# Kernel optimization log

Measured on AMD Instinct MI355X. Metric: run time of the kernel, lower is better.

Reference implementation:

```python
import jax, jax.numpy as jnp
import numpy as np

B, C, H, W = 64, 256, 16, 16
HEADS, HEAD_DIM = 8, 256            # NOTE: source code requires H*W == HEAD_DIM
HID = HEADS * HEAD_DIM              # 2048
TEMB = 512
EPS = 1e-6
SC = HEAD_DIM ** -0.5


def setup_inputs() -> dict:
    key = jax.random.key(0)
    ks = jax.random.split(key, 6)
    return {
        "x": jax.random.normal(ks[0], (B, C, H, W), jnp.float32),
        "time_emb": jax.random.normal(ks[1], (B, TEMB), jnp.float32),
        "mlp_w": jax.random.normal(ks[2], (2 * C, TEMB), jnp.float32) * 0.02,
        "mlp_b": jnp.zeros((2 * C,), jnp.float32),
        "qkv_w": jax.random.normal(ks[3], (3 * HID, C), jnp.float32) * 0.02,
        "out_w": jax.random.normal(ks[4], (C, HID), jnp.float32) * 0.02,
        "out_b": jnp.zeros((C,), jnp.float32),
        "out_norm_scale": jnp.ones((C,), jnp.float32),
    }


def reference(x, time_emb, mlp_w, mlp_b, qkv_w, out_w, out_b, out_norm_scale):
    # AdaRMSNorm: SiLU -> Linear -> per-batch (scale, shift) over channels
    ss = jax.nn.silu(time_emb) @ mlp_w.T + mlp_b          # [B, 2C]
    scale, shift = jnp.split(ss, 2, axis=1)
    scale = scale[:, :, None, None]
    shift = shift[:, :, None, None]
    inv = jax.lax.rsqrt(jnp.mean(x * x, axis=1, keepdims=True) + EPS)
    xn = x * inv * (1.0 + scale) + shift

    # 1x1 conv producing q,k,v
    qkv = jnp.einsum('bchw,oc->bohw', xn, qkv_w)          # [B, 3*HID, H, W]
    q, k, v = jnp.split(qkv, 3, axis=1)

    def to_heads(t):
        return t.reshape(B, HEADS, HEAD_DIM, H * W)       # [B, h, d, L]

    q = jax.nn.softmax(to_heads(q), axis=2) * SC          # softmax over head_dim
    k = jax.nn.softmax(to_heads(k), axis=3)               # softmax over spatial
    v = to_heads(v)

    # Faithful to source einsums (contract over head_dim c, then over c and lw1)
    ctx = jnp.einsum('bhcn,bhcm->bhnm', k, v) * SC        # [B, h, L, L]
    out = jnp.einsum('bhnm,bhcl->bhml', ctx, q)           # [B, h, L, L]

    # rearrange 'b h c (l w) -> b (h c) l w' (valid since L == HEAD_DIM)
    out = out.reshape(B, HID, H, W)

    # output 1x1 conv + RMSNorm + residual
    y = jnp.einsum('bohw,co->bchw', out, out_w) + out_b[None, :, None, None]
    inv2 = jax.lax.rsqrt(jnp.mean(y * y, axis=1, keepdims=True) + EPS)
    y = y * inv2 * out_norm_scale[None, :, None, None]
    return y + x
```

## Files before the change

kernel.cpp:

```cpp
#include <hip/hip_runtime.h>
#include <math.h>


static constexpr float EPSV = 1e-6f;
static constexpr float SC2 = 1.0f / 256.0f;

__device__ __forceinline__ float wave_sum(float v) {
    v += __shfl_xor(v, 1);  v += __shfl_xor(v, 2);
    v += __shfl_xor(v, 4);  v += __shfl_xor(v, 8);
    v += __shfl_xor(v, 16); v += __shfl_xor(v, 32);
    return v;
}

__global__ void __launch_bounds__(256) k0_prep(
    const float* __restrict__ temb, const float* __restrict__ mlp_w,
    const float* __restrict__ mlp_b, const float* __restrict__ qkv_w,
    float* __restrict__ scsh, float* __restrict__ wvg)
{
    const int blk = blockIdx.x, tid = threadIdx.x;
    const int wv = tid >> 6, lane = tid & 63;
    if (blk < 1024) {
        int b = blk >> 4, jg = blk & 15;
        __shared__ float sl[512];
        float v0 = temb[b * 512 + tid];
        float v1 = temb[b * 512 + 256 + tid];
        sl[tid] = v0 / (1.0f + expf(-v0));
        sl[256 + tid] = v1 / (1.0f + expf(-v1));
        __syncthreads();
        int j0 = jg * 32 + wv * 8;
        float acc[8] = {0, 0, 0, 0, 0, 0, 0, 0};
        const float* wb = mlp_w + (size_t)j0 * 512 + lane;
#pragma unroll
        for (int k = 0; k < 8; ++k) {
            float sv = sl[k * 64 + lane];
#pragma unroll
            for (int jj = 0; jj < 8; ++jj)
                acc[jj] = fmaf(wb[(size_t)jj * 512 + k * 64], sv, acc[jj]);
        }
#pragma unroll
        for (int jj = 0; jj < 8; ++jj) {
            float a = wave_sum(acc[jj]);
            if (lane == 0) scsh[b * 512 + j0 + jj] = a + mlp_b[j0 + jj];
        }
    } else {
        int w = blk - 1024;
        int h = w >> 2, cq = w & 3;
        __shared__ float sm[256];
        const float* base =
            qkv_w + (size_t)(4096 + h * 256 + wv * 64) * 256 + cq * 64 + lane;
        float s = 0.f;
#pragma unroll 8
        for (int r = 0; r < 64; ++r) s += base[(size_t)r * 256];
        sm[wv * 64 + lane] = s;
        __syncthreads();
        if (tid < 64)
            wvg[h * 256 + cq * 64 + tid] =
                sm[tid] + sm[64 + tid] + sm[128 + tid] + sm[192 + tid];
    }
}

__global__ void __launch_bounds__(1024) k1_body(
    const float* __restrict__ x, const float* __restrict__ scsh,
    const float* __restrict__ wvg, const float* __restrict__ out_w,
    float* __restrict__ ypart)
{
    const int blk = blockIdx.x, tid = threadIdx.x;
    const int wv = tid >> 6, lane = tid & 63;
    const int b = blk >> 2, q = blk & 3;

    __shared__ float coef[256 * 8];
    __shared__ float apart[16 * 64 * 9];
    __shared__ float finbuf[64 * 9];
    __shared__ float ofl[512];
    __shared__ float ssh[8];
    __shared__ float parts[8 * 4];

    {
        int c = tid & 255, hp = tid >> 8;
        float sc = 1.0f + scsh[b * 512 + c];
        float sh = scsh[b * 512 + 256 + c];
#pragma unroll
        for (int e = 0; e < 2; ++e) {
            int h = hp * 2 + e;
            float wvv = wvg[h * 256 + c];
            coef[c * 8 + h] = sc * wvv;
            float sv = wave_sum(sh * wvv);
            if (lane == 0) parts[h * 4 + (wv & 3)] = sv;
        }
    }
    __syncthreads();
    if (tid < 8)
        ssh[tid] = parts[tid * 4 + 0] + parts[tid * 4 + 1] +
                   parts[tid * 4 + 2] + parts[tid * 4 + 3];

    {
        int m = tid & 63, cg = tid >> 6;
        float A[8] = {0, 0, 0, 0, 0, 0, 0, 0};
        float ss2 = 0.f;
        const float* xb = x + (size_t)b * 65536 + q * 64 + m;
#pragma unroll
        for (int ci = 0; ci < 16; ++ci) {
            int c = cg * 16 + ci;
            float xv = xb[(size_t)c * 256];
            ss2 = fmaf(xv, xv, ss2);
            const float4 c0 = *reinterpret_cast<const float4*>(&coef[c * 8]);
            const float4 c1 = *reinterpret_cast<const float4*>(&coef[c * 8 + 4]);
            A[0] = fmaf(xv, c0.x, A[0]); A[1] = fmaf(xv, c0.y, A[1]);
            A[2] = fmaf(xv, c0.z, A[2]); A[3] = fmaf(xv, c0.w, A[3]);
            A[4] = fmaf(xv, c1.x, A[4]); A[5] = fmaf(xv, c1.y, A[5]);
            A[6] = fmaf(xv, c1.z, A[6]); A[7] = fmaf(xv, c1.w, A[7]);
        }
        float* ap = apart + ((size_t)cg * 64 + m) * 9;
#pragma unroll
        for (int h = 0; h < 8; ++h) ap[h] = A[h];
        ap[8] = ss2;
    }
    __syncthreads();

    if (tid < 576) {
        int m = tid & 63, i = tid >> 6;
        float s = 0.f;
#pragma unroll
        for (int cg = 0; cg < 16; ++cg)
            s += apart[((size_t)cg * 64 + m) * 9 + i];
        finbuf[m * 9 + i] = s;
    }
    __syncthreads();

    if (tid < 512) {
        int h = tid >> 6, m = tid & 63;
        float inv = rsqrtf(finbuf[m * 9 + 8] * (1.0f / 256.0f) + EPSV);
        ofl[h * 64 + m] = SC2 * fmaf(inv, finbuf[m * 9 + h], ssh[h]);
    }
    __syncthreads();

    {
        const float4* of4 = reinterpret_cast<const float4*>(ofl);
#pragma unroll
        for (int g4 = 0; g4 < 4; ++g4) {
            int c0 = wv * 16 + g4 * 4;
            float a[4] = {0, 0, 0, 0};
#pragma unroll
            for (int cc = 0; cc < 4; ++cc) {
                int c = c0 + cc;
#pragma unroll
                for (int k = 0; k < 2; ++k) {
                    int idx = k * 64 + lane;
                    int h = idx >> 4, mm = (idx & 15) * 4;
                    const float4 w4 = *reinterpret_cast<const float4*>(
                        &out_w[(size_t)c * 2048 + h * 256 + q * 64 + mm]);
                    float4 ov = of4[idx];
                    a[cc] = fmaf(w4.x, ov.x, a[cc]);
                    a[cc] = fmaf(w4.y, ov.y, a[cc]);
                    a[cc] = fmaf(w4.z, ov.z, a[cc]);
                    a[cc] = fmaf(w4.w, ov.w, a[cc]);
                }
            }
#pragma unroll
            for (int cc = 0; cc < 4; ++cc) {
                float s = wave_sum(a[cc]);
                if (lane == 0)
                    ypart[(size_t)q * 16384 + b * 256 + c0 + cc] = s;
            }
        }
    }
}

__global__ void __launch_bounds__(1024) k2_fin(
    const float* __restrict__ ypart, const float* __restrict__ out_b,
    const float* __restrict__ onorm, const float* __restrict__ x,
    float* __restrict__ out)
{
    const int blk = blockIdx.x, tid = threadIdx.x;
    const int b = blk >> 3, ch = blk & 7;
    __shared__ float gl[256];
    __shared__ float wred[4];
    if (tid < 256) {
        float yb = out_b[tid] +
                   ypart[b * 256 + tid] + ypart[16384 + b * 256 + tid] +
                   ypart[32768 + b * 256 + tid] + ypart[49152 + b * 256 + tid];
        float v2 = wave_sum(yb * yb);
        if ((tid & 63) == 0) wred[tid >> 6] = v2;
        gl[tid] = yb;
    }
    __syncthreads();
    {
        float inv2 = rsqrtf((wred[0] + wred[1] + wred[2] + wred[3]) *
                            (1.0f / 256.0f) + EPSV);
        if (tid < 256) gl[tid] = gl[tid] * inv2 * onorm[tid];
    }
    __syncthreads();

    const float4* xx = reinterpret_cast<const float4*>(x) +
                       (size_t)b * 16384 + ch * 2048;
    float4* oo = reinterpret_cast<float4*>(out) + (size_t)b * 16384 + ch * 2048;
#pragma unroll
    for (int k = 0; k < 2; ++k) {
        int i = k * 1024 + tid;
        int row = (ch * 2048 + i) >> 6;
        float4 xv = xx[i];
        float gg = gl[row];
        oo[i] = make_float4(xv.x + gg, xv.y + gg, xv.z + gg, xv.w + gg);
    }
}

extern "C" void kernel_launch(void* const* d_in, const int* in_sizes, int n_in,
                              void* d_out, int out_size, void* d_ws, size_t ws_size,
                              hipStream_t stream) {
    const float* x     = (const float*)d_in[0];
    const float* temb  = (const float*)d_in[1];
    const float* mlp_w = (const float*)d_in[2];
    const float* mlp_b = (const float*)d_in[3];
    const float* qkv_w = (const float*)d_in[4];
    const float* out_w = (const float*)d_in[5];
    const float* out_b = (const float*)d_in[6];
    const float* onorm = (const float*)d_in[7];
    float* out = (float*)d_out;
    float* ws  = (float*)d_ws;

    float* scsh  = ws;
    float* wvg   = ws + 32768;
    float* ypart = ws + 34816;

    k0_prep<<<1056, 256,  0, stream>>>(temb, mlp_w, mlp_b, qkv_w, scsh, wvg);
    k1_body<<<256,  1024, 0, stream>>>(x, scsh, wvg, out_w, ypart);
    k2_fin <<<512,  1024, 0, stream>>>(ypart, out_b, onorm, x, out);
}
```

Before: 31.93 us.

## Vectorize x loads in body kernel and prefetch x before reductions

The body kernel now has each thread load four float4 values of x at the very start, before the coefficient setup. It accumulates 8 head projections plus the sum of squares for 4 spatial positions per thread, then reduces across lanes with shuffles before the shared-memory reduction. The finalize kernel also issues its x loads before the norm computation so their latency overlaps the reduction. The aim is to cut scalar global-load count and hide memory latency, at the cost of more registers (36 accumulators) and extra shuffles.

Result: slower. 35.88 us (+12.4%).

```diff
diff --git a/kernel.cpp b/kernel.cpp
--- a/kernel.cpp
+++ b/kernel.cpp
@@ -67,13 +67,21 @@
     const int blk = blockIdx.x, tid = threadIdx.x;
     const int wv = tid >> 6, lane = tid & 63;
     const int b = blk >> 2, q = blk & 3;
+    const int m4 = tid & 15, cg = tid >> 4;
 
     __shared__ float coef[256 * 8];
-    __shared__ float apart[16 * 64 * 9];
-    __shared__ float finbuf[64 * 9];
+    __shared__ float apart[256 * 36];
+    __shared__ float finbuf[16 * 36];
     __shared__ float ofl[512];
     __shared__ float ssh[8];
     __shared__ float parts[8 * 4];
+
+    const float4* x4 = reinterpret_cast<const float4*>(x) +
+                       (size_t)b * 16384 + q * 16 + m4;
+    float4 xr0 = x4[(size_t)(cg * 4 + 0) * 64];
+    float4 xr1 = x4[(size_t)(cg * 4 + 1) * 64];
+    float4 xr2 = x4[(size_t)(cg * 4 + 2) * 64];
+    float4 xr3 = x4[(size_t)(cg * 4 + 3) * 64];
 
     {
         int c = tid & 255, hp = tid >> 8;
@@ -94,43 +102,55 @@
                    parts[tid * 4 + 2] + parts[tid * 4 + 3];
 
     {
-        int m = tid & 63, cg = tid >> 6;
-        float A[8] = {0, 0, 0, 0, 0, 0, 0, 0};
-        float ss2 = 0.f;
-        const float* xb = x + (size_t)b * 65536 + q * 64 + m;
-#pragma unroll
-        for (int ci = 0; ci < 16; ++ci) {
-            int c = cg * 16 + ci;
-            float xv = xb[(size_t)c * 256];
-            ss2 = fmaf(xv, xv, ss2);
+        float acc[36];
+#pragma unroll
+        for (int i = 0; i < 36; ++i) acc[i] = 0.f;
+        float4 xa[4] = {xr0, xr1, xr2, xr3};
+#pragma unroll
+        for (int ci = 0; ci < 4; ++ci) {
+            int c = cg * 4 + ci;
+            float xm[4] = {xa[ci].x, xa[ci].y, xa[ci].z, xa[ci].w};
             const float4 c0 = *reinterpret_cast<const float4*>(&coef[c * 8]);
             const float4 c1 = *reinterpret_cast<const float4*>(&coef[c * 8 + 4]);
-            A[0] = fmaf(xv, c0.x, A[0]); A[1] = fmaf(xv, c0.y, A[1]);
-            A[2] = fmaf(xv, c0.z, A[2]); A[3] = fmaf(xv, c0.w, A[3]);
-            A[4] = fmaf(xv, c1.x, A[4]); A[5] = fmaf(xv, c1.y, A[5]);
-            A[6] = fmaf(xv, c1.z, A[6]); A[7] = fmaf(xv, c1.w, A[7]);
-        }
-        float* ap = apart + ((size_t)cg * 64 + m) * 9;
-#pragma unroll
-        for (int h = 0; h < 8; ++h) ap[h] = A[h];
-        ap[8] = ss2;
+            float cf[8] = {c0.x, c0.y, c0.z, c0.w, c1.x, c1.y, c1.z, c1.w};
+#pragma unroll
+            for (int h = 0; h < 8; ++h)
+#pragma unroll
+                for (int mi = 0; mi < 4; ++mi)
+                    acc[h * 4 + mi] = fmaf(xm[mi], cf[h], acc[h * 4 + mi]);
+#pragma unroll
+            for (int mi = 0; mi < 4; ++mi)
+                acc[32 + mi] = fmaf(xm[mi], xm[mi], acc[32 + mi]);
+        }
+#pragma unroll
+        for (int i = 0; i < 36; ++i) {
+            acc[i] += __shfl_xor(acc[i], 16);
+            acc[i] += __shfl_xor(acc[i], 32);
+        }
+        if (lane < 16) {
+#pragma unroll
+            for (int i = 0; i < 36; ++i)
+                apart[((size_t)wv * 16 + lane) * 36 + i] = acc[i];
+        }
     }
     __syncthreads();
 
     if (tid < 576) {
-        int m = tid & 63, i = tid >> 6;
+        int i = tid >> 4, m4r = tid & 15;
         float s = 0.f;
 #pragma unroll
-        for (int cg = 0; cg < 16; ++cg)
-            s += apart[((size_t)cg * 64 + m) * 9 + i];
-        finbuf[m * 9 + i] = s;
+        for (int w = 0; w < 16; ++w)
+            s += apart[((size_t)w * 16 + m4r) * 36 + i];
+        finbuf[m4r * 36 + i] = s;
     }
     __syncthreads();
 
     if (tid < 512) {
-        int h = tid >> 6, m = tid & 63;
-        float inv = rsqrtf(finbuf[m * 9 + 8] * (1.0f / 256.0f) + EPSV);
-        ofl[h * 64 + m] = SC2 * fmaf(inv, finbuf[m * 9 + h], ssh[h]);
+        int h = tid >> 6, mm = tid & 63;
+        int m4r = mm >> 2, mi = mm & 3;
+        float inv = rsqrtf(finbuf[m4r * 36 + 32 + mi] * (1.0f / 256.0f) + EPSV);
+        ofl[h * 64 + mm] = SC2 * fmaf(inv, finbuf[m4r * 36 + h * 4 + mi],
+                                      ssh[h]);
     }
     __syncthreads();
 
@@ -175,6 +195,12 @@
     const int b = blk >> 3, ch = blk & 7;
     __shared__ float gl[256];
     __shared__ float wred[4];
+
+    const float4* xx = reinterpret_cast<const float4*>(x) +
+                       (size_t)b * 16384 + ch * 2048;
+    float4 xr0 = xx[tid];
+    float4 xr1 = xx[1024 + tid];
+
     if (tid < 256) {
         float yb = out_b[tid] +
                    ypart[b * 256 + tid] + ypart[16384 + b * 256 + tid] +
@@ -191,16 +217,15 @@
     }
     __syncthreads();
 
-    const float4* xx = reinterpret_cast<const float4*>(x) +
-                       (size_t)b * 16384 + ch * 2048;
     float4* oo = reinterpret_cast<float4*>(out) + (size_t)b * 16384 + ch * 2048;
-#pragma unroll
-    for (int k = 0; k < 2; ++k) {
-        int i = k * 1024 + tid;
-        int row = (ch * 2048 + i) >> 6;
-        float4 xv = xx[i];
-        float gg = gl[row];
-        oo[i] = make_float4(xv.x + gg, xv.y + gg, xv.z + gg, xv.w + gg);
+    {
+        int row0 = (ch * 2048 + tid) >> 6;
+        float g0 = gl[row0];
+        oo[tid] = make_float4(xr0.x + g0, xr0.y + g0, xr0.z + g0, xr0.w + g0);
+        int row1 = (ch * 2048 + 1024 + tid) >> 6;
+        float g1 = gl[row1];
+        oo[1024 + tid] =
+            make_float4(xr1.x + g1, xr1.y + g1, xr1.z + g1, xr1.w + g1);
     }
 }
 
```
